# Kernel tuning notes

Measured on AMD Instinct MI355X. Metric: run time of the kernel, lower is better.

Reference implementation:

```python
import jax, jax.numpy as jnp
import numpy as np

INDIM, HID, OUTDIM, T = 28, 128, 10, 28

def setup_inputs() -> dict:
    key = jax.random.key(0)
    ks = jax.random.split(key, 7)
    B = 65536
    bound1 = 1.0 / np.sqrt(INDIM)
    bound2 = 1.0 / np.sqrt(2 * HID)
    bound3 = 1.0 / np.sqrt(HID)
    return {
        "x": jax.random.normal(ks[0], (B, 784), dtype=jnp.float32),
        "W1": jax.random.uniform(ks[1], (INDIM, HID), jnp.float32, -bound1, bound1),
        "b1": jax.random.uniform(ks[2], (HID,), jnp.float32, -bound1, bound1),
        "W2": jax.random.uniform(ks[3], (2 * HID, HID), jnp.float32, -bound2, bound2),
        "b2": jax.random.uniform(ks[4], (HID,), jnp.float32, -bound2, bound2),
        "W3": jax.random.uniform(ks[5], (HID, OUTDIM), jnp.float32, -bound3, bound3),
        "b3": jax.random.uniform(ks[6], (OUTDIM,), jnp.float32, -bound3, bound3),
    }

def reference(x, W1, b1, W2, b2, W3, b3):
    B = x.shape[0]
    # (B, 784) -> (T, B, 28): scan over the 28 rows of each image
    rows = jnp.transpose(x.reshape(B, T, INDIM), (1, 0, 2))
    # W2 split: first HID rows multiply linear1 output, last HID rows multiply hidden state
    W2a, W2b = W2[:HID], W2[HID:]

    def step(h, row):
        t = row @ W1 + b1                      # (B, HID)
        h_new = jax.nn.relu(t @ W2a + h @ W2b + b2)  # concat(t, h) @ W2 == t@W2a + h@W2b
        return h_new, None

    h0 = jnp.zeros((B, HID), dtype=x.dtype)
    h_final, _ = jax.lax.scan(step, h0, rows)
    return h_final @ W3 + b3
```

## Files before the change

### kernel.cpp

```cpp
#include <hip/hip_runtime.h>

#define BTOT 65536
#define TST  28
#define PACK_DW 100
#define WXL_OFF 12800

typedef __attribute__((ext_vector_type(8))) short bf16x8;
typedef __attribute__((ext_vector_type(4))) float f32x4;
typedef __attribute__((ext_vector_type(2))) unsigned int u32x2;

__device__ __forceinline__ unsigned int f2bf(float f) {
    unsigned u = __float_as_uint(f);
    u += 0x7fff + ((u >> 16) & 1);
    return u >> 16;
}
__device__ __forceinline__ unsigned int pk2bf(float a, float b) {
    return f2bf(a) | (f2bf(b) << 16);
}
__device__ __forceinline__ bf16x8 cvt8(f32x4 a, f32x4 b) {
    union { unsigned int u[4]; bf16x8 v; } r;
    asm("v_cvt_pk_bf16_f32 %0, %1, %2" : "=v"(r.u[0]) : "v"(a[0]), "v"(a[1]));
    asm("v_cvt_pk_bf16_f32 %0, %1, %2" : "=v"(r.u[1]) : "v"(a[2]), "v"(a[3]));
    asm("v_cvt_pk_bf16_f32 %0, %1, %2" : "=v"(r.u[2]) : "v"(b[0]), "v"(b[1]));
    asm("v_cvt_pk_bf16_f32 %0, %1, %2" : "=v"(r.u[3]) : "v"(b[2]), "v"(b[3]));
    return r.v;
}

__global__ void pack1(const float* __restrict__ W1, const float* __restrict__ b1,
                      const float* __restrict__ W2, const float* __restrict__ b2,
                      const float* __restrict__ W3, const float* __restrict__ b3,
                      unsigned int* __restrict__ ws) {
    float* WxL = (float*)(ws + WXL_OFF);
    const int bid = blockIdx.x, tid = threadIdx.x;
    if (bid < 29) {
        const int k = bid, n = tid;
        float s = 0.f;
        if (k < 28) {
            for (int m = 0; m < 128; ++m) s += W1[k * 128 + m] * W2[m * 128 + n];
        } else {
            s = b2[n];
            for (int m = 0; m < 128; ++m) s += b1[m] * W2[m * 128 + n];
        }
        WxL[k * 128 + n] = s;
        if (k == 28) { WxL[29*128+n] = 0.f; WxL[30*128+n] = 0.f; WxL[31*128+n] = 0.f; }
    } else if (bid == 29) {
        if (tid < 64) {
            const int lr = tid & 15, kh = tid >> 4;
            for (int p = 0; p < 2; ++p) {
                unsigned int* P = ws + (p * 64 + tid) * PACK_DW;
                for (int kk = 0; kk < 4; ++kk)
                    for (int t = 0; t < 4; ++t)
                        for (int jd = 0; jd < 4; ++jd) {
                            const int k = 128 + kk * 32 + kh * 8 + jd * 2;
                            const int n = p * 64 + t * 16 + lr;
                            P[(kk * 4 + t) * 4 + jd] =
                                pk2bf(W2[k * 128 + n], W2[(k + 1) * 128 + n]);
                        }
            }
        }
    } else {
        if (tid < 64) {
            const int lr = tid & 15, kh = tid >> 4;
            unsigned int* P = ws + tid * PACK_DW;
            for (int kk = 0; kk < 4; ++kk)
                for (int jd = 0; jd < 4; ++jd) {
                    const int k = kk * 32 + kh * 8 + jd * 2;
                    float lo = (lr < 10) ? W3[k * 10 + lr] : 0.f;
                    float hi = (lr < 10) ? W3[(k + 1) * 10 + lr] : 0.f;
                    P[80 + kk * 4 + jd] = pk2bf(lo, hi);
                }
            for (int j = 0; j < 4; ++j) {
                const int o = kh * 4 + j;
                P[96 + j] = __float_as_uint((o < 10) ? b3[o] : 0.f);
            }
        }
    }
}

__global__ void pack2(unsigned int* __restrict__ ws) {
    const int tid = threadIdx.x;
    if (tid < 64) {
        const float* WxL = (const float*)(ws + WXL_OFF);
        const int lr = tid & 15, kh = tid >> 4;
        for (int p = 0; p < 2; ++p) {
            unsigned int* P = ws + (p * 64 + tid) * PACK_DW;
            for (int t = 0; t < 4; ++t)
                for (int jd = 0; jd < 4; ++jd) {
                    const int k = kh * 8 + jd * 2, n = p * 64 + t * 16 + lr;
                    P[64 + t * 4 + jd] = pk2bf(WxL[k * 128 + n], WxL[(k + 1) * 128 + n]);
                }
        }
    }
}

__global__ __launch_bounds__(256, 3) void rnn_kernel(
    const float* __restrict__ x, const unsigned int* __restrict__ wsPack,
    float* __restrict__ out)
{
    __shared__ __align__(16) unsigned int Hs[2][2][1024];
    const int tid = threadIdx.x;
    const int w = tid >> 6, lane = tid & 63, lr = lane & 15, kh = lane >> 4;
    const int g = w >> 1, p = w & 1;
    const int r0 = blockIdx.x * 32 + g * 16;

    const unsigned int* P = wsPack + (p * 64 + lane) * PACK_DW;
    bf16x8 w2b[4][4], wx[4];
    #pragma unroll
    for (int kk = 0; kk < 4; ++kk)
        #pragma unroll
        for (int t = 0; t < 4; ++t)
            w2b[kk][t] = *(const bf16x8*)(P + (kk * 4 + t) * 4);
    #pragma unroll
    for (int t = 0; t < 4; ++t) wx[t] = *(const bf16x8*)(P + 64 + t * 4);

    unsigned wAddr[4];
    #pragma unroll
    for (int t4 = 0; t4 < 4; ++t4) {
        const int kkW = p * 2 + (t4 >> 1);
        const int khR = (t4 * 2 + (kh >> 1)) & 3;
        const int jd  = (kh & 1) * 2;
        wAddr[t4] = kkW * 256 + khR * 64 + lr * 4 + jd;
    }

    #pragma unroll
    for (int i = 0; i < 4; ++i) {
        Hs[0][0][tid + i * 256] = 0u;
        Hs[1][0][tid + i * 256] = 0u;
    }
    __syncthreads();

    const f32x4 onec = {1.f, 0.f, 0.f, 0.f};
    const float* xr = x + (size_t)(r0 + lr) * 784 + 8 * kh;
    f32x4 xa = *(const f32x4*)xr;
    f32x4 xc = (kh < 3) ? *(const f32x4*)(xr + 4) : onec;
    bf16x8 xb = cvt8(xa, xc);
    const f32x4 z4 = {0.f, 0.f, 0.f, 0.f};

    int cur = 0;
    for (int t = 0; t < TST; ++t) {
        f32x4 na, nc;
        const bool pf = (t + 1 < TST);
        if (pf) {
            const float* xp = xr + (t + 1) * 28;
            na = *(const f32x4*)xp;
            nc = (kh < 3) ? *(const f32x4*)(xp + 4) : onec;
        }

        f32x4 acc[4];
        #pragma unroll
        for (int t4 = 0; t4 < 4; ++t4)
            acc[t4] = __builtin_amdgcn_mfma_f32_16x16x32_bf16(wx[t4], xb, z4, 0, 0, 0);
        bf16x8 hbv[4];
        #pragma unroll
        for (int kk = 0; kk < 4; ++kk)
            hbv[kk] = *(const bf16x8*)&Hs[g][cur][kk * 256 + lane * 4];
        #pragma unroll
        for (int kk = 0; kk < 4; ++kk)
            #pragma unroll
            for (int t4 = 0; t4 < 4; ++t4)
                acc[t4] = __builtin_amdgcn_mfma_f32_16x16x32_bf16(w2b[kk][t4], hbv[kk], acc[t4], 0, 0, 0);
        #pragma unroll
        for (int t4 = 0; t4 < 4; ++t4) {
            f32x4 v = acc[t4];
            v[0] = fmaxf(v[0], 0.f); v[1] = fmaxf(v[1], 0.f);
            v[2] = fmaxf(v[2], 0.f); v[3] = fmaxf(v[3], 0.f);
            unsigned lo, hi;
            asm("v_cvt_pk_bf16_f32 %0, %1, %2" : "=v"(lo) : "v"(v[0]), "v"(v[1]));
            asm("v_cvt_pk_bf16_f32 %0, %1, %2" : "=v"(hi) : "v"(v[2]), "v"(v[3]));
            u32x2 st = {lo, hi};
            *(u32x2*)&Hs[g][cur ^ 1][wAddr[t4]] = st;
        }
        if (pf) xb = cvt8(na, nc);
        asm volatile("s_waitcnt lgkmcnt(0)\n\ts_barrier" ::: "memory");
        cur ^= 1;
    }

    if (p == 0) {
        bf16x8 w3f[4];
        #pragma unroll
        for (int kk = 0; kk < 4; ++kk) w3f[kk] = *(const bf16x8*)(P + 80 + kk * 4);
        const float* bp = (const float*)(P + 96);
        f32x4 accO = {bp[0], bp[1], bp[2], bp[3]};
        #pragma unroll
        for (int kk = 0; kk < 4; ++kk) {
            bf16x8 hb = *(const bf16x8*)&Hs[g][cur][kk * 256 + lane * 4];
            accO = __builtin_amdgcn_mfma_f32_16x16x32_bf16(w3f[kk], hb, accO, 0, 0, 0);
        }
        float* op = out + (size_t)(r0 + lr) * 10 + kh * 4;
        #pragma unroll
        for (int j = 0; j < 4; ++j)
            if (kh * 4 + j < 10) op[j] = accO[j];
    }
}

extern "C" void kernel_launch(void* const* d_in, const int* in_sizes, int n_in,
                              void* d_out, int out_size, void* d_ws, size_t ws_size,
                              hipStream_t stream) {
    const float* x  = (const float*)d_in[0];
    const float* W1 = (const float*)d_in[1];
    const float* b1 = (const float*)d_in[2];
    const float* W2 = (const float*)d_in[3];
    const float* b2 = (const float*)d_in[4];
    const float* W3 = (const float*)d_in[5];
    const float* b3 = (const float*)d_in[6];
    unsigned int* ws = (unsigned int*)d_ws;

    pack1<<<31, 128, 0, stream>>>(W1, b1, W2, b2, W3, b3, ws);
    pack2<<<1, 64, 0, stream>>>(ws);
    rnn_kernel<<<BTOT / 32, 256, 0, stream>>>(x, ws, (float*)d_out);
}
```

Measured before the change: 79.40 us.

## Process two 16-row batch tiles per wave to reuse register-held weights

Shrinks the block to two waves, with each wave computing both 16-row batch groups, so the resident W2b and Wx register fragments feed twice as many MFMAs per step. The aim is to halve the per-block weight register loading and barrier participants and to interleave two independent MFMA chains, hiding MFMA latency within a wave. In exchange each wave holds more accumulators and hidden-state fragments, which raises register pressure. Launch bounds change to 128 threads with a lower occupancy hint.

```diff
diff --git a/kernel.cpp b/kernel.cpp
--- a/kernel.cpp
+++ b/kernel.cpp
@@ -93,15 +93,14 @@
     }
 }
 
-__global__ __launch_bounds__(256, 3) void rnn_kernel(
+__global__ __launch_bounds__(128, 2) void rnn_kernel(
     const float* __restrict__ x, const unsigned int* __restrict__ wsPack,
     float* __restrict__ out)
 {
     __shared__ __align__(16) unsigned int Hs[2][2][1024];
     const int tid = threadIdx.x;
-    const int w = tid >> 6, lane = tid & 63, lr = lane & 15, kh = lane >> 4;
-    const int g = w >> 1, p = w & 1;
-    const int r0 = blockIdx.x * 32 + g * 16;
+    const int p = tid >> 6, lane = tid & 63, lr = lane & 15, kh = lane >> 4;
+    const int r0 = blockIdx.x * 32;
 
     const unsigned int* P = wsPack + (p * 64 + lane) * PACK_DW;
     bf16x8 w2b[4][4], wx[4];
@@ -123,54 +122,75 @@
     }
 
     #pragma unroll
-    for (int i = 0; i < 4; ++i) {
-        Hs[0][0][tid + i * 256] = 0u;
-        Hs[1][0][tid + i * 256] = 0u;
+    for (int i = 0; i < 8; ++i) {
+        Hs[0][0][tid + i * 128] = 0u;
+        Hs[1][0][tid + i * 128] = 0u;
     }
     __syncthreads();
 
     const f32x4 onec = {1.f, 0.f, 0.f, 0.f};
-    const float* xr = x + (size_t)(r0 + lr) * 784 + 8 * kh;
-    f32x4 xa = *(const f32x4*)xr;
-    f32x4 xc = (kh < 3) ? *(const f32x4*)(xr + 4) : onec;
-    bf16x8 xb = cvt8(xa, xc);
+    const float* xrA = x + (size_t)(r0 + lr) * 784 + 8 * kh;
+    const float* xrB = xrA + 16 * 784;
+    f32x4 qa = *(const f32x4*)xrA;
+    f32x4 qc = (kh < 3) ? *(const f32x4*)(xrA + 4) : onec;
+    bf16x8 xbA = cvt8(qa, qc);
+    qa = *(const f32x4*)xrB;
+    qc = (kh < 3) ? *(const f32x4*)(xrB + 4) : onec;
+    bf16x8 xbB = cvt8(qa, qc);
     const f32x4 z4 = {0.f, 0.f, 0.f, 0.f};
 
     int cur = 0;
     for (int t = 0; t < TST; ++t) {
-        f32x4 na, nc;
+        f32x4 naA, ncA, naB, ncB;
         const bool pf = (t + 1 < TST);
         if (pf) {
-            const float* xp = xr + (t + 1) * 28;
-            na = *(const f32x4*)xp;
-            nc = (kh < 3) ? *(const f32x4*)(xp + 4) : onec;
-        }
-
-        f32x4 acc[4];
-        #pragma unroll
-        for (int t4 = 0; t4 < 4; ++t4)
-            acc[t4] = __builtin_amdgcn_mfma_f32_16x16x32_bf16(wx[t4], xb, z4, 0, 0, 0);
-        bf16x8 hbv[4];
-        #pragma unroll
-        for (int kk = 0; kk < 4; ++kk)
-            hbv[kk] = *(const bf16x8*)&Hs[g][cur][kk * 256 + lane * 4];
+            const float* xp = xrA + (t + 1) * 28;
+            naA = *(const f32x4*)xp;
+            ncA = (kh < 3) ? *(const f32x4*)(xp + 4) : onec;
+            xp = xrB + (t + 1) * 28;
+            naB = *(const f32x4*)xp;
+            ncB = (kh < 3) ? *(const f32x4*)(xp + 4) : onec;
+        }
+
+        bf16x8 hbvA[4], hbvB[4];
+        #pragma unroll
+        for (int kk = 0; kk < 4; ++kk) {
+            hbvA[kk] = *(const bf16x8*)&Hs[0][cur][kk * 256 + lane * 4];
+            hbvB[kk] = *(const bf16x8*)&Hs[1][cur][kk * 256 + lane * 4];
+        }
+
+        f32x4 accA[4], accB[4];
+        #pragma unroll
+        for (int t4 = 0; t4 < 4; ++t4) {
+            accA[t4] = __builtin_amdgcn_mfma_f32_16x16x32_bf16(wx[t4], xbA, z4, 0, 0, 0);
+            accB[t4] = __builtin_amdgcn_mfma_f32_16x16x32_bf16(wx[t4], xbB, z4, 0, 0, 0);
+        }
         #pragma unroll
         for (int kk = 0; kk < 4; ++kk)
             #pragma unroll
-            for (int t4 = 0; t4 < 4; ++t4)
-                acc[t4] = __builtin_amdgcn_mfma_f32_16x16x32_bf16(w2b[kk][t4], hbv[kk], acc[t4], 0, 0, 0);
+            for (int t4 = 0; t4 < 4; ++t4) {
+                accA[t4] = __builtin_amdgcn_mfma_f32_16x16x32_bf16(w2b[kk][t4], hbvA[kk], accA[t4], 0, 0, 0);
+                accB[t4] = __builtin_amdgcn_mfma_f32_16x16x32_bf16(w2b[kk][t4], hbvB[kk], accB[t4], 0, 0, 0);
+            }
+
         #pragma unroll
         for (int t4 = 0; t4 < 4; ++t4) {
-            f32x4 v = acc[t4];
-            v[0] = fmaxf(v[0], 0.f); v[1] = fmaxf(v[1], 0.f);
-            v[2] = fmaxf(v[2], 0.f); v[3] = fmaxf(v[3], 0.f);
+            f32x4 va = accA[t4], vb = accB[t4];
+            va[0] = fmaxf(va[0], 0.f); va[1] = fmaxf(va[1], 0.f);
+            va[2] = fmaxf(va[2], 0.f); va[3] = fmaxf(va[3], 0.f);
+            vb[0] = fmaxf(vb[0], 0.f); vb[1] = fmaxf(vb[1], 0.f);
+            vb[2] = fmaxf(vb[2], 0.f); vb[3] = fmaxf(vb[3], 0.f);
             unsigned lo, hi;
-            asm("v_cvt_pk_bf16_f32 %0, %1, %2" : "=v"(lo) : "v"(v[0]), "v"(v[1]));
-            asm("v_cvt_pk_bf16_f32 %0, %1, %2" : "=v"(hi) : "v"(v[2]), "v"(v[3]));
-            u32x2 st = {lo, hi};
-            *(u32x2*)&Hs[g][cur ^ 1][wAddr[t4]] = st;
-        }
-        if (pf) xb = cvt8(na, nc);
+            asm("v_cvt_pk_bf16_f32 %0, %1, %2" : "=v"(lo) : "v"(va[0]), "v"(va[1]));
+            asm("v_cvt_pk_bf16_f32 %0, %1, %2" : "=v"(hi) : "v"(va[2]), "v"(va[3]));
+            u32x2 stA = {lo, hi};
+            *(u32x2*)&Hs[0][cur ^ 1][wAddr[t4]] = stA;
+            asm("v_cvt_pk_bf16_f32 %0, %1, %2" : "=v"(lo) : "v"(vb[0]), "v"(vb[1]));
+            asm("v_cvt_pk_bf16_f32 %0, %1, %2" : "=v"(hi) : "v"(vb[2]), "v"(vb[3]));
+            u32x2 stB = {lo, hi};
+            *(u32x2*)&Hs[1][cur ^ 1][wAddr[t4]] = stB;
+        }
+        if (pf) { xbA = cvt8(naA, ncA); xbB = cvt8(naB, ncB); }
         asm volatile("s_waitcnt lgkmcnt(0)\n\ts_barrier" ::: "memory");
         cur ^= 1;
     }
@@ -180,16 +200,19 @@
         #pragma unroll
         for (int kk = 0; kk < 4; ++kk) w3f[kk] = *(const bf16x8*)(P + 80 + kk * 4);
         const float* bp = (const float*)(P + 96);
-        f32x4 accO = {bp[0], bp[1], bp[2], bp[3]};
-        #pragma unroll
-        for (int kk = 0; kk < 4; ++kk) {
-            bf16x8 hb = *(const bf16x8*)&Hs[g][cur][kk * 256 + lane * 4];
-            accO = __builtin_amdgcn_mfma_f32_16x16x32_bf16(w3f[kk], hb, accO, 0, 0, 0);
-        }
-        float* op = out + (size_t)(r0 + lr) * 10 + kh * 4;
-        #pragma unroll
-        for (int j = 0; j < 4; ++j)
-            if (kh * 4 + j < 10) op[j] = accO[j];
+        #pragma unroll
+        for (int g = 0; g < 2; ++g) {
+            f32x4 accO = {bp[0], bp[1], bp[2], bp[3]};
+            #pragma unroll
+            for (int kk = 0; kk < 4; ++kk) {
+                bf16x8 hb = *(const bf16x8*)&Hs[g][cur][kk * 256 + lane * 4];
+                accO = __builtin_amdgcn_mfma_f32_16x16x32_bf16(w3f[kk], hb, accO, 0, 0, 0);
+            }
+            float* op = out + (size_t)(r0 + g * 16 + lr) * 10 + kh * 4;
+            #pragma unroll
+            for (int j = 0; j < 4; ++j)
+                if (kh * 4 + j < 10) op[j] = accO[j];
+        }
     }
 }
 
@@ -207,5 +230,5 @@
 
     pack1<<<31, 128, 0, stream>>>(W1, b1, W2, b2, W3, b3, ws);
     pack2<<<1, 64, 0, stream>>>(ws);
-    rnn_kernel<<<BTOT / 32, 256, 0, stream>>>(x, ws, (float*)d_out);
-}
+    rnn_kernel<<<BTOT / 32, 128, 0, stream>>>(x, ws, (float*)d_out);
+}
```

Result: slower. 84.29 us (+6.2%).
